# Kernel optimization log

Measured on AMD Instinct MI355X. Metric: run time of the kernel, lower is better.

The kernel has to match this reference:

```python
import jax, jax.numpy as jnp
import numpy as np

N = 50000      # nodes
E = 1600000    # edges
CIN = 64
COUT = 64
U = 3
V = 3


def setup_inputs() -> dict:
    key = jax.random.key(0)
    k1, k2, k3, k4 = jax.random.split(key, 4)
    featureTensor = jax.random.normal(k1, (N, CIN), dtype=jnp.float32)
    neighborhoodTensor = jax.random.randint(k2, (2, E), 0, N, dtype=jnp.int64)
    filterTensor = jax.random.uniform(k3, (E, U, V), dtype=jnp.float32)
    # xavier_normal-ish init for the [u, v, Cin, Cout] weight tensor
    std = float(np.sqrt(2.0 / (CIN + COUT)))
    weight = jax.random.normal(k4, (U, V, CIN, COUT), dtype=jnp.float32) * std
    return {
        "featureTensor": featureTensor,
        "neighborhoodTensor": neighborhoodTensor,
        "filterTensor": filterTensor,
        "weight": weight,
    }


def reference(featureTensor, neighborhoodTensor, filterTensor, weight):
    # meshLayer.forward with dense_for_center=False, bias=False, activation=None:
    # out[n] = sum_{e: row0[e]==n} einsum('i,uv,uvio->o', x[row1[e]], filt[e], W)
    row, col = neighborhoodTensor[0], neighborhoodTensor[1]
    x_j = featureTensor[col]                      # [E, Cin] gather of source features
    ff = filterTensor.reshape(E, U * V)           # [E, K] with K = u*v = 9
    Wf = weight.reshape(U * V, CIN, COUT)         # [K, Cin, Cout]
    # small fixed loop over K=9 basis slots keeps peak memory at [E, Cout]
    msg = ff[:, 0, None] * (x_j @ Wf[0])
    for k in range(1, U * V):
        msg = msg + ff[:, k, None] * (x_j @ Wf[k])
    out = jax.ops.segment_sum(msg, row, num_segments=N)  # scatter-add to nodes
    return out
```

## Files before the change

kernel.cpp:

```cpp
#include <hip/hip_runtime.h>


#define CH 64
#define KB 9
#define LROW 584

using f32x4  = __attribute__((ext_vector_type(4))) float;
using bf16x8 = __attribute__((ext_vector_type(8))) short;

__device__ __forceinline__ float bf2f(unsigned short u) {
    unsigned v = ((unsigned)u) << 16;
    return __builtin_bit_cast(float, v);
}
__device__ __forceinline__ unsigned short f2bf(float f) {
    unsigned x = __builtin_bit_cast(unsigned, f);
    unsigned r = (x + 0x7FFFu + ((x >> 16) & 1u)) >> 16;
    return (unsigned short)r;
}
__device__ __forceinline__ float lo16(unsigned v) {
    return __builtin_bit_cast(float, v << 16);
}
__device__ __forceinline__ float hi16(unsigned v) {
    return __builtin_bit_cast(float, v & 0xFFFF0000u);
}
__device__ __forceinline__ unsigned pk(float a, float b) {
    return (unsigned)f2bf(a) | ((unsigned)f2bf(b) << 16);
}


__global__ void k_hist_xconv(const int* __restrict__ row, int* __restrict__ cnt,
                             const float* __restrict__ x, unsigned short* __restrict__ xb,
                             int E, int Nn) {
    int stride = gridDim.x * blockDim.x;
    int gid = blockIdx.x * blockDim.x + threadIdx.x;
    for (int e = gid; e < E; e += stride) {
        int r = row[e];
        r = (r < 0) ? 0 : ((r >= Nn) ? Nn - 1 : r);
        atomicAdd(&cnt[r], 1);
    }
    int M = Nn * CH;
    for (int i = gid; i < M; i += stride) xb[i] = f2bf(x[i]);
}

__global__ void k_scan1(const int* __restrict__ cnt, int* __restrict__ loc,
                        int* __restrict__ csum, int Nn) {
    int t = threadIdx.x, lane = t & 63, w = t >> 6;
    int i = blockIdx.x * 256 + t;
    int v = (i < Nn) ? cnt[i] : 0;
    int x = v;
#pragma unroll
    for (int off = 1; off < 64; off <<= 1) {
        int y = __shfl_up(x, off);
        if (lane >= off) x += y;
    }
    __shared__ int ws[4], wo[4];
    if (lane == 63) ws[w] = x;
    __syncthreads();
    if (t == 0) {
        int s = 0;
        for (int j = 0; j < 4; j++) { int tv = ws[j]; wo[j] = s; s += tv; }
    }
    __syncthreads();
    x += wo[w];
    if (i < Nn) loc[i] = x - v;
    if (t == 255) csum[blockIdx.x] = x;
}

__global__ void k_scan2(const int* __restrict__ csum, int* __restrict__ coff, int nch) {
    int t = threadIdx.x, lane = t & 63, w = t >> 6;
    int v = (t < nch) ? csum[t] : 0;
    int x = v;
#pragma unroll
    for (int off = 1; off < 64; off <<= 1) {
        int y = __shfl_up(x, off);
        if (lane >= off) x += y;
    }
    __shared__ int ws[4], wo[4];
    if (lane == 63) ws[w] = x;
    __syncthreads();
    if (t == 0) {
        int s = 0;
        for (int j = 0; j < 4; j++) { int tv = ws[j]; wo[j] = s; s += tv; }
    }
    __syncthreads();
    x += wo[w];
    if (t < nch) coff[t] = x - v;
}

__global__ void k_scan3_wprep(const int* __restrict__ loc, const int* __restrict__ coff,
                              int* __restrict__ starts, int* __restrict__ cur,
                              const float* __restrict__ W, unsigned short* __restrict__ wfb,
                              int Nn, int E) {
    int i = blockIdx.x * 256 + threadIdx.x;
    if (i < Nn) {
        int st = loc[i] + coff[i >> 8];
        starts[i] = st;
        cur[i] = st;
    }
    if (i == 0) starts[Nn] = E;
    if (i < 72 * 64) {
        int f = i >> 6, lane = i & 63;
        int kstep = f >> 2, cb = f & 3;
        int q0 = kstep * 32 + (lane >> 4) * 8;
        int c = cb * 16 + (lane & 15);
        unsigned short* dst = wfb + (size_t)i * 8;
#pragma unroll
        for (int j = 0; j < 8; j++) dst[j] = f2bf(W[(q0 + j) * CH + c]);
    }
}

__global__ void k_scatter(const int* __restrict__ row, const int* __restrict__ col,
                          const float* __restrict__ ff, int* __restrict__ cur,
                          unsigned* __restrict__ rec, int E, int Nn) {
    int stride = gridDim.x * blockDim.x;
    for (int e = blockIdx.x * blockDim.x + threadIdx.x; e < E; e += stride) {
        int r = row[e];
        r = (r < 0) ? 0 : ((r >= Nn) ? Nn - 1 : r);
        int c = col[e];
        c = (c < 0) ? 0 : ((c >= Nn) ? Nn - 1 : c);
        const float* fp = ff + (size_t)e * KB;
        unsigned d1 = pk(fp[0], fp[1]);
        unsigned d2 = pk(fp[2], fp[3]);
        unsigned d3 = pk(fp[4], fp[5]);
        unsigned d4 = pk(fp[6], fp[7]);
        unsigned d5 = (unsigned)f2bf(fp[8]);
        int pos = atomicAdd(&cur[r], 1);
        uint4* dst = (uint4*)(rec + (size_t)pos * 8);
        uint4 a, b;
        a.x = (unsigned)c; a.y = d1; a.z = d2; a.w = d3;
        b.x = d4; b.y = d5; b.z = 0u; b.w = 0u;
        dst[0] = a;
        dst[1] = b;
    }
}


#define FMA9(ra, rb, xv)                                   \
    acc0 = fmaf(lo16((ra).y), (xv), acc0);                 \
    acc1 = fmaf(hi16((ra).y), (xv), acc1);                 \
    acc2 = fmaf(lo16((ra).z), (xv), acc2);                 \
    acc3 = fmaf(hi16((ra).z), (xv), acc3);                 \
    acc4 = fmaf(lo16((ra).w), (xv), acc4);                 \
    acc5 = fmaf(hi16((ra).w), (xv), acc5);                 \
    acc6 = fmaf(lo16((rb).x), (xv), acc6);                 \
    acc7 = fmaf(hi16((rb).x), (xv), acc7);                 \
    acc8 = fmaf(lo16((rb).y), (xv), acc8);

__global__ __launch_bounds__(256) void k_fused(const unsigned short* __restrict__ xb,
                                               const unsigned* __restrict__ rec,
                                               const int* __restrict__ starts,
                                               const unsigned short* __restrict__ wfb,
                                               float* __restrict__ out, int Nn) {
    __shared__ unsigned short A[16 * LROW];
    int t = threadIdx.x, w = t >> 6, lane = t & 63;
    int n0 = blockIdx.x * 16;

    for (int j = 0; j < 4; ++j) {
        int node = n0 + w * 4 + j;
        float acc0 = 0, acc1 = 0, acc2 = 0, acc3 = 0, acc4 = 0,
              acc5 = 0, acc6 = 0, acc7 = 0, acc8 = 0;
        if (node < Nn) {
            int s = starts[node], e = starts[node + 1];
            const uint4* r4 = (const uint4*)rec + (size_t)s * 2;
            int m = e - s, p = 0;
            for (; p + 4 <= m; p += 4) {
                uint4 ra0 = r4[p * 2 + 0], rb0 = r4[p * 2 + 1];
                uint4 ra1 = r4[p * 2 + 2], rb1 = r4[p * 2 + 3];
                uint4 ra2 = r4[p * 2 + 4], rb2 = r4[p * 2 + 5];
                uint4 ra3 = r4[p * 2 + 6], rb3 = r4[p * 2 + 7];
                float x0 = bf2f(xb[ra0.x * CH + lane]);
                float x1 = bf2f(xb[ra1.x * CH + lane]);
                float x2 = bf2f(xb[ra2.x * CH + lane]);
                float x3 = bf2f(xb[ra3.x * CH + lane]);
                FMA9(ra0, rb0, x0)
                FMA9(ra1, rb1, x1)
                FMA9(ra2, rb2, x2)
                FMA9(ra3, rb3, x3)
            }
            for (; p < m; ++p) {
                uint4 ra = r4[p * 2 + 0], rb = r4[p * 2 + 1];
                float xv = bf2f(xb[ra.x * CH + lane]);
                FMA9(ra, rb, xv)
            }
        }
        unsigned short* dst = A + (w * 4 + j) * LROW + lane;
        dst[0 * 64] = f2bf(acc0); dst[1 * 64] = f2bf(acc1); dst[2 * 64] = f2bf(acc2);
        dst[3 * 64] = f2bf(acc3); dst[4 * 64] = f2bf(acc4); dst[5 * 64] = f2bf(acc5);
        dst[6 * 64] = f2bf(acc6); dst[7 * 64] = f2bf(acc7); dst[8 * 64] = f2bf(acc8);
    }
    __syncthreads();

    f32x4 C = {0, 0, 0, 0};
    int arow = lane & 15, g = lane >> 4;
    const unsigned short* ab = A + arow * LROW + g * 8;
    const bf16x8* wv = (const bf16x8*)wfb;
#pragma unroll
    for (int ks = 0; ks < 18; ++ks) {
        bf16x8 a = *(const bf16x8*)(ab + ks * 32);
        bf16x8 b = wv[(ks * 4 + w) * 64 + lane];
        C = __builtin_amdgcn_mfma_f32_16x16x32_bf16(a, b, C, 0, 0, 0);
    }
    float* ob = out + (size_t)n0 * CH + w * 16 + (lane & 15);
#pragma unroll
    for (int r = 0; r < 4; ++r) {
        int orow = g * 4 + r;
        if (n0 + orow < Nn) ob[orow * CH] = C[r];
    }
}

extern "C" void kernel_launch(void* const* d_in, const int* in_sizes, int n_in,
                              void* d_out, int out_size, void* d_ws, size_t ws_size,
                              hipStream_t stream) {
    const float* x   = (const float*)d_in[0];
    const int*   nbr = (const int*)d_in[1];
    const float* ff  = (const float*)d_in[2];
    const float* W   = (const float*)d_in[3];
    float* out = (float*)d_out;

    int Nn = in_sizes[0] / CH;
    int E  = in_sizes[1] / 2;
    const int* row = nbr;
    const int* col = nbr + E;

    char* p = (char*)d_ws;
    auto alloc = [&](size_t bytes) -> void* {
        void* r = (void*)p;
        p += (bytes + 511) & ~(size_t)511;
        return r;
    };
    int* cnt    = (int*)alloc((size_t)Nn * 4);
    int* loc    = (int*)alloc((size_t)Nn * 4);
    int* csum   = (int*)alloc(1024);
    int* coff   = (int*)alloc(1024);
    int* starts = (int*)alloc((size_t)(Nn + 1) * 4);
    int* cur    = (int*)alloc((size_t)Nn * 4);
    unsigned* rec = (unsigned*)alloc((size_t)E * 32);
    unsigned short* xb  = (unsigned short*)alloc((size_t)Nn * CH * 2);
    unsigned short* wfb = (unsigned short*)alloc(72 * 64 * 8 * 2);

    hipMemsetAsync(cnt, 0, (size_t)Nn * 4, stream);

    k_hist_xconv<<<2048, 256, 0, stream>>>(row, cnt, x, xb, E, Nn);

    int nch = (Nn + 255) / 256;
    k_scan1<<<nch, 256, 0, stream>>>(cnt, loc, csum, Nn);
    k_scan2<<<1, 256, 0, stream>>>(csum, coff, nch);
    k_scan3_wprep<<<nch, 256, 0, stream>>>(loc, coff, starts, cur, W, wfb, Nn, E);

    k_scatter<<<2048, 256, 0, stream>>>(row, col, ff, cur, rec, E, Nn);

    k_fused<<<(Nn + 15) / 16, 256, 0, stream>>>(xb, rec, starts, wfb, out, Nn);
}
```

Baseline: 398.7 us.

## Stream edge records into LDS via async DMA with triple-buffered pipelined gathers

The fused aggregation kernel now treats each wave's four nodes as one contiguous edge segment. It prefetches 64-record chunks into a triple-buffered LDS region using global_load_lds DMA, and software-pipelines the record reads and feature gathers in batches of four, flushing accumulators at node boundaries. The scatter kernel switches to nontemporal stores, and launch bounds request three blocks per CU. The aim is to hide record-load latency and raise memory-level parallelism, at the cost of more LDS use, hand-placed waitcnt instructions and extra control-flow complexity.

```diff
diff --git a/kernel.cpp b/kernel.cpp
--- a/kernel.cpp
+++ b/kernel.cpp
@@ -6,7 +6,10 @@
 #define LROW 584
 
 using f32x4  = __attribute__((ext_vector_type(4))) float;
+using f32x2  = __attribute__((ext_vector_type(2))) float;
 using bf16x8 = __attribute__((ext_vector_type(8))) short;
+using u32x4  = __attribute__((ext_vector_type(4))) unsigned;
+using u32x2  = __attribute__((ext_vector_type(2))) unsigned;
 
 __device__ __forceinline__ float bf2f(unsigned short u) {
     unsigned v = ((unsigned)u) << 16;
@@ -23,8 +26,13 @@
 __device__ __forceinline__ float hi16(unsigned v) {
     return __builtin_bit_cast(float, v & 0xFFFF0000u);
 }
-__device__ __forceinline__ unsigned pk(float a, float b) {
+__device__ __forceinline__ unsigned pkbf(float a, float b) {
     return (unsigned)f2bf(a) | ((unsigned)f2bf(b) << 16);
+}
+__device__ __forceinline__ void dma16(const void* g, void* l) {
+    __builtin_amdgcn_global_load_lds(
+        (const __attribute__((address_space(1))) unsigned int*)g,
+        (__attribute__((address_space(3))) unsigned int*)l, 16, 0, 0);
 }
 
 
@@ -119,91 +127,155 @@
         int c = col[e];
         c = (c < 0) ? 0 : ((c >= Nn) ? Nn - 1 : c);
         const float* fp = ff + (size_t)e * KB;
-        unsigned d1 = pk(fp[0], fp[1]);
-        unsigned d2 = pk(fp[2], fp[3]);
-        unsigned d3 = pk(fp[4], fp[5]);
-        unsigned d4 = pk(fp[6], fp[7]);
-        unsigned d5 = (unsigned)f2bf(fp[8]);
+        u32x4 v0, v1;
+        v0.x = (unsigned)c;
+        v0.y = pkbf(fp[0], fp[1]);
+        v0.z = pkbf(fp[2], fp[3]);
+        v0.w = pkbf(fp[4], fp[5]);
+        v1.x = pkbf(fp[6], fp[7]);
+        v1.y = (unsigned)f2bf(fp[8]);
+        v1.z = 0u; v1.w = 0u;
         int pos = atomicAdd(&cur[r], 1);
-        uint4* dst = (uint4*)(rec + (size_t)pos * 8);
-        uint4 a, b;
-        a.x = (unsigned)c; a.y = d1; a.z = d2; a.w = d3;
-        b.x = d4; b.y = d5; b.z = 0u; b.w = 0u;
-        dst[0] = a;
-        dst[1] = b;
-    }
-}
-
-
-#define FMA9(ra, rb, xv)                                   \
-    acc0 = fmaf(lo16((ra).y), (xv), acc0);                 \
-    acc1 = fmaf(hi16((ra).y), (xv), acc1);                 \
-    acc2 = fmaf(lo16((ra).z), (xv), acc2);                 \
-    acc3 = fmaf(hi16((ra).z), (xv), acc3);                 \
-    acc4 = fmaf(lo16((ra).w), (xv), acc4);                 \
-    acc5 = fmaf(hi16((ra).w), (xv), acc5);                 \
-    acc6 = fmaf(lo16((rb).x), (xv), acc6);                 \
-    acc7 = fmaf(hi16((rb).x), (xv), acc7);                 \
-    acc8 = fmaf(lo16((rb).y), (xv), acc8);
-
-__global__ __launch_bounds__(256) void k_fused(const unsigned short* __restrict__ xb,
-                                               const unsigned* __restrict__ rec,
-                                               const int* __restrict__ starts,
-                                               const unsigned short* __restrict__ wfb,
-                                               float* __restrict__ out, int Nn) {
-    __shared__ unsigned short A[16 * LROW];
+        u32x4* dst = (u32x4*)(rec + (size_t)pos * 8);
+        __builtin_nontemporal_store(v0, dst);
+        __builtin_nontemporal_store(v1, dst + 1);
+    }
+}
+
+
+struct RecT { u32x4 a; u32x2 b; };
+
+__global__ __launch_bounds__(256, 3) void k_fused(const unsigned short* __restrict__ xb,
+                                                  const unsigned* __restrict__ rec,
+                                                  const int* __restrict__ starts,
+                                                  const unsigned short* __restrict__ wfb,
+                                                  float* __restrict__ out, int Nn) {
+    __shared__ unsigned short Ash[16 * LROW];
+    __shared__ u32x4 recbuf[3 * 4 * 128];
     int t = threadIdx.x, w = t >> 6, lane = t & 63;
     int n0 = blockIdx.x * 16;
-
-    for (int j = 0; j < 4; ++j) {
-        int node = n0 + w * 4 + j;
-        float acc0 = 0, acc1 = 0, acc2 = 0, acc3 = 0, acc4 = 0,
-              acc5 = 0, acc6 = 0, acc7 = 0, acc8 = 0;
-        if (node < Nn) {
-            int s = starts[node], e = starts[node + 1];
-            const uint4* r4 = (const uint4*)rec + (size_t)s * 2;
-            int m = e - s, p = 0;
-            for (; p + 4 <= m; p += 4) {
-                uint4 ra0 = r4[p * 2 + 0], rb0 = r4[p * 2 + 1];
-                uint4 ra1 = r4[p * 2 + 2], rb1 = r4[p * 2 + 3];
-                uint4 ra2 = r4[p * 2 + 4], rb2 = r4[p * 2 + 5];
-                uint4 ra3 = r4[p * 2 + 6], rb3 = r4[p * 2 + 7];
-                float x0 = bf2f(xb[ra0.x * CH + lane]);
-                float x1 = bf2f(xb[ra1.x * CH + lane]);
-                float x2 = bf2f(xb[ra2.x * CH + lane]);
-                float x3 = bf2f(xb[ra3.x * CH + lane]);
-                FMA9(ra0, rb0, x0)
-                FMA9(ra1, rb1, x1)
-                FMA9(ra2, rb2, x2)
-                FMA9(ra3, rb3, x3)
+    int nb = n0 + w * 4;
+    int w4 = w * 4;
+
+    int segS = starts[nb];
+    int bnd0 = starts[nb + 1];
+    int bnd1 = starts[nb + 2];
+    int bnd2 = starts[nb + 3];
+    int segE = starts[nb + 4];
+
+    f32x2 a01 = (f32x2)(0.0f), a23 = (f32x2)(0.0f), a45 = (f32x2)(0.0f), a67 = (f32x2)(0.0f);
+    float a8 = 0.0f;
+    int cnode = 0;
+    int nextBnd = bnd0;
+
+    auto flushNode = [&]() {
+        unsigned short* d = &Ash[(w4 + cnode) * LROW + lane];
+        d[0]   = f2bf(a01.x); d[64]  = f2bf(a01.y);
+        d[128] = f2bf(a23.x); d[192] = f2bf(a23.y);
+        d[256] = f2bf(a45.x); d[320] = f2bf(a45.y);
+        d[384] = f2bf(a67.x); d[448] = f2bf(a67.y);
+        d[512] = f2bf(a8);
+        a01 = (f32x2)(0.0f); a23 = (f32x2)(0.0f);
+        a45 = (f32x2)(0.0f); a67 = (f32x2)(0.0f); a8 = 0.0f;
+        ++cnode;
+        nextBnd = (cnode == 1) ? bnd1 : (cnode == 2) ? bnd2 : segE;
+    };
+
+    auto edge = [&](const RecT& r, unsigned short xvv, int q) {
+        if (q < segE) {
+            while (q == nextBnd) flushNode();
+            float xf = bf2f(xvv);
+            f32x2 xf2 = {xf, xf};
+            f32x2 pr;
+            pr.x = lo16(r.a.y); pr.y = hi16(r.a.y); a01 += pr * xf2;
+            pr.x = lo16(r.a.z); pr.y = hi16(r.a.z); a23 += pr * xf2;
+            pr.x = lo16(r.a.w); pr.y = hi16(r.a.w); a45 += pr * xf2;
+            pr.x = lo16(r.b.x); pr.y = hi16(r.b.x); a67 += pr * xf2;
+            a8 = fmaf(lo16(r.b.y), xf, a8);
+        }
+    };
+
+    auto dmaChunk = [&](int cc) {
+        const char* gs = (const char*)rec + ((size_t)(segS + (cc << 6))) * 32 + lane * 16;
+        char* ls = (char*)recbuf + (((cc % 3) * 4 + w) * 2048);
+        dma16(gs, ls);
+        dma16(gs + 1024, ls + 1024);
+    };
+
+    if (segS < segE) {
+        int m = segE - segS;
+        int nchunks = (m + 63) >> 6;
+        dmaChunk(0);
+        if (nchunks > 1) dmaChunk(1);
+        for (int c = 0; c < nchunks; ++c) {
+            if (c == 0) {
+                if (nchunks > 1) { asm volatile("s_waitcnt vmcnt(2)" ::: "memory"); }
+                else             { asm volatile("s_waitcnt vmcnt(0)" ::: "memory"); }
+            } else {
+                asm volatile("s_waitcnt vmcnt(6)" ::: "memory");
             }
-            for (; p < m; ++p) {
-                uint4 ra = r4[p * 2 + 0], rb = r4[p * 2 + 1];
-                float xv = bf2f(xb[ra.x * CH + lane]);
-                FMA9(ra, rb, xv)
+            __builtin_amdgcn_sched_barrier(0);
+            const char* rb = (const char*)recbuf + (((c % 3) * 4 + w) * 2048);
+            int base = segS + (c << 6);
+            int lim = segE - base; if (lim > 64) lim = 64;
+            int nbat = (lim + 3) >> 2;
+
+            auto readRec = [&](int idx) {
+                RecT r;
+                r.a = *(const u32x4*)(rb + (idx & 63) * 32);
+                r.b = *(const u32x2*)(rb + (idx & 63) * 32 + 16);
+                return r;
+            };
+            auto gather4 = [&](const RecT* rr, unsigned short* xv) {
+#pragma unroll
+                for (int j = 0; j < 4; ++j) {
+                    unsigned cc_ = rr[j].a.x;
+                    cc_ = (cc_ < (unsigned)Nn) ? cc_ : 0u;
+                    xv[j] = xb[(size_t)cc_ * CH + lane];
+                }
+            };
+
+            RecT r0[4], r1[4];
+            unsigned short xv0[4], xv1[4];
+#pragma unroll
+            for (int j = 0; j < 4; ++j) r0[j] = readRec(j);
+            gather4(r0, xv0);
+
+            int b = 0;
+            while (true) {
+                if (b == 2 && c + 2 < nchunks) dmaChunk(c + 2);
+#pragma unroll
+                for (int j = 0; j < 4; ++j) r1[j] = readRec((b + 1) * 4 + j);
+                gather4(r1, xv1);
+#pragma unroll
+                for (int j = 0; j < 4; ++j) edge(r0[j], xv0[j], base + b * 4 + j);
+                if (++b >= nbat) break;
+#pragma unroll
+                for (int j = 0; j < 4; ++j) r0[j] = readRec((b + 1) * 4 + j);
+                gather4(r0, xv0);
+#pragma unroll
+                for (int j = 0; j < 4; ++j) edge(r1[j], xv1[j], base + b * 4 + j);
+                if (++b >= nbat) break;
             }
         }
-        unsigned short* dst = A + (w * 4 + j) * LROW + lane;
-        dst[0 * 64] = f2bf(acc0); dst[1 * 64] = f2bf(acc1); dst[2 * 64] = f2bf(acc2);
-        dst[3 * 64] = f2bf(acc3); dst[4 * 64] = f2bf(acc4); dst[5 * 64] = f2bf(acc5);
-        dst[6 * 64] = f2bf(acc6); dst[7 * 64] = f2bf(acc7); dst[8 * 64] = f2bf(acc8);
-    }
+    }
+    while (cnode < 4) flushNode();
     __syncthreads();
 
     f32x4 C = {0, 0, 0, 0};
-    int arow = lane & 15, g = lane >> 4;
-    const unsigned short* ab = A + arow * LROW + g * 8;
+    int arow = lane & 15, g2 = lane >> 4;
+    const unsigned short* ab = Ash + arow * LROW + g2 * 8;
     const bf16x8* wv = (const bf16x8*)wfb;
 #pragma unroll
     for (int ks = 0; ks < 18; ++ks) {
         bf16x8 a = *(const bf16x8*)(ab + ks * 32);
-        bf16x8 b = wv[(ks * 4 + w) * 64 + lane];
-        C = __builtin_amdgcn_mfma_f32_16x16x32_bf16(a, b, C, 0, 0, 0);
+        bf16x8 bfr = wv[(ks * 4 + w) * 64 + lane];
+        C = __builtin_amdgcn_mfma_f32_16x16x32_bf16(a, bfr, C, 0, 0, 0);
     }
     float* ob = out + (size_t)n0 * CH + w * 16 + (lane & 15);
 #pragma unroll
     for (int r = 0; r < 4; ++r) {
-        int orow = g * 4 + r;
+        int orow = g2 * 4 + r;
         if (n0 + orow < Nn) ob[orow * CH] = C[r];
     }
 }
@@ -234,11 +306,11 @@
     int* coff   = (int*)alloc(1024);
     int* starts = (int*)alloc((size_t)(Nn + 1) * 4);
     int* cur    = (int*)alloc((size_t)Nn * 4);
-    unsigned* rec = (unsigned*)alloc((size_t)E * 32);
+    unsigned* rec = (unsigned*)alloc((size_t)E * 32 + 4096);
     unsigned short* xb  = (unsigned short*)alloc((size_t)Nn * CH * 2);
     unsigned short* wfb = (unsigned short*)alloc(72 * 64 * 8 * 2);
 
-    hipMemsetAsync(cnt, 0, (size_t)Nn * 4, stream);
+    (void)hipMemsetAsync(cnt, 0, (size_t)Nn * 4, stream);
 
     k_hist_xconv<<<2048, 256, 0, stream>>>(row, cnt, x, xb, E, Nn);
 
```

Result: slower. 1.135 ms (+184.6%).
